# Performance work log

Hardware: AMD Instinct MI355X
Metric: run time of the kernel (lower is better)

Reference implementation:

```python
import jax, jax.numpy as jnp
import numpy as np

N_TOKENS = 16384
D_MODEL = 1024
N_EXPERTS = 4
TOP_K = 2
LN_EPS = 1e-6


def setup_inputs() -> dict:
    key = jax.random.key(0)
    ks = jax.random.split(key, 6)
    d, e = D_MODEL, N_EXPERTS
    return {
        "x": jax.random.normal(ks[0], (N_TOKENS, d), jnp.float32),
        "gate_w": jax.random.normal(ks[1], (e, d), jnp.float32) * (1.0 / np.sqrt(d)),
        "w1": jax.random.normal(ks[2], (e, 2 * d, d), jnp.float32) * (1.0 / np.sqrt(d)),
        "b1": jax.random.normal(ks[3], (e, 2 * d), jnp.float32) * 0.01,
        "w2": jax.random.normal(ks[4], (e, d, 2 * d), jnp.float32) * (1.0 / np.sqrt(2 * d)),
        "b2": jax.random.normal(ks[5], (e, d), jnp.float32) * 0.01,
        "gamma": jnp.ones((e, d), jnp.float32),
        "beta": jnp.zeros((e, d), jnp.float32),
    }


def _expert_ffn(x, w1e, b1e, w2e, b2e, ge, be):
    h = jax.nn.gelu(x @ w1e.T + b1e, approximate=False)   # [N, 2d]
    z = x + (h @ w2e.T + b2e)                              # residual, [N, d]
    mu = jnp.mean(z, axis=-1, keepdims=True)
    var = jnp.var(z, axis=-1, keepdims=True)
    return (z - mu) * jax.lax.rsqrt(var + LN_EPS) * ge + be


def reference(x, gate_w, w1, b1, w2, b2, gamma, beta):
    n = x.shape[0]
    scores = x @ gate_w.T                                  # [N, E]
    ew, ei = jax.lax.top_k(scores, TOP_K)                  # [N, K]
    ew = jax.nn.softmax(ew, axis=-1)
    # combine weights: dense [N, E] routing matrix (each row has K nonzeros)
    comb = jnp.zeros_like(scores).at[jnp.arange(n)[:, None], ei].add(ew)
    y = jnp.zeros_like(x)
    for e in range(N_EXPERTS):  # small fixed expert count
        y = y + comb[:, e:e + 1] * _expert_ffn(x, w1[e], b1[e], w2[e], b2[e], gamma[e], beta[e])
    return y
```

## Files before the change

### kernel.cpp

```cpp
#include <hip/hip_runtime.h>
#include <hip/hip_bf16.h>
#include <math.h>

#define NT 16384
#define DM 1024
#define NE 4

typedef __attribute__((ext_vector_type(8))) short short8;
typedef __attribute__((ext_vector_type(4))) float f32x4;

#define GLDS(g, l)                                                        \
  __builtin_amdgcn_global_load_lds(                                       \
      (const __attribute__((address_space(1))) void*)(g),                 \
      (__attribute__((address_space(3))) void*)(l), 16, 0, 0)

__device__ __forceinline__ float bf2f(short h) {
    union { unsigned u; float f; } v;
    v.u = ((unsigned)(unsigned short)h) << 16;
    return v.f;
}

__global__ __launch_bounds__(256) void detect_kernel(
    const unsigned int* __restrict__ xw, int* __restrict__ flag)
{
    __shared__ int red[4];
    const int t = threadIdx.x;
    int cnt = 0;
    #pragma unroll 4
    for (int i = 0; i < 64; ++i) {
        unsigned w = xw[t * 64 + i];
        unsigned e0 = (w >> 7) & 0xFFu;
        cnt += (e0 >= 100u && e0 <= 150u) ? 1 : 0;
    }
    #pragma unroll
    for (int o = 32; o > 0; o >>= 1) cnt += __shfl_xor(cnt, o);
    if ((t & 63) == 0) red[t >> 6] = cnt;
    __syncthreads();
    if (t == 0) {
        int tot = red[0] + red[1] + red[2] + red[3];
        *flag = (tot > 8192) ? 1 : 0;
    }
}

__global__ __launch_bounds__(256) void init_kernel(
    int* __restrict__ counts, int* __restrict__ idx)
{
    const int t = blockIdx.x * 256 + threadIdx.x;
    idx[t] = 0;
    if (t < NE) counts[t] = 0;
}

__global__ __launch_bounds__(256) void convert_big_kernel(
    const float* __restrict__ src, short* __restrict__ dst, int n,
    const int* __restrict__ flag)
{
    if (*flag) return;
    const int stride = gridDim.x * blockDim.x;
    const int t0 = blockIdx.x * blockDim.x + threadIdx.x;
    const float4* s = (const float4*)src;
    for (int i = t0; i < n / 4; i += stride) {
        float4 v = s[i];
        __hip_bfloat16 b0 = __float2bfloat16(v.x);
        __hip_bfloat16 b1 = __float2bfloat16(v.y);
        __hip_bfloat16 b2 = __float2bfloat16(v.z);
        __hip_bfloat16 b3 = __float2bfloat16(v.w);
        short4 o;
        o.x = *(short*)&b0; o.y = *(short*)&b1;
        o.z = *(short*)&b2; o.w = *(short*)&b3;
        *(short4*)(dst + (size_t)i * 4) = o;
    }
}

__global__ __launch_bounds__(256) void convert_small_kernel(
    const void* __restrict__ b1, const void* __restrict__ b2,
    const void* __restrict__ ga, const void* __restrict__ be,
    short* __restrict__ b1d, short* __restrict__ b2d,
    short* __restrict__ gad, short* __restrict__ bed,
    const int* __restrict__ flag)
{
    const int isbf = *flag;
    const int t = blockIdx.x * 256 + threadIdx.x;
    const void* src; short* dst; int i;
    if (t < 8192)      { src = b1; dst = b1d; i = t; }
    else if (t < 12288){ src = b2; dst = b2d; i = t - 8192; }
    else if (t < 16384){ src = ga; dst = gad; i = t - 12288; }
    else               { src = be; dst = bed; i = t - 16384; }
    short v;
    if (isbf) v = ((const short*)src)[i];
    else {
        __hip_bfloat16 b = __float2bfloat16(((const float*)src)[i]);
        v = *(short*)&b;
    }
    dst[i] = v;
}

__global__ __launch_bounds__(256) void gate_kernel(
    const void* __restrict__ x, const void* __restrict__ gw,
    float* __restrict__ comb, int* __restrict__ choice,
    const int* __restrict__ flag)
{
    const int lane  = threadIdx.x & 63;
    const int token = blockIdx.x * 4 + (threadIdx.x >> 6);
    double s0 = 0., s1 = 0., s2 = 0., s3 = 0.;
    if (*flag) {
        const short8* xr = (const short8*)((const short*)x + (size_t)token * DM);
        const short8* g0 = (const short8*)((const short*)gw + 0 * DM);
        const short8* g1 = (const short8*)((const short*)gw + 1 * DM);
        const short8* g2 = (const short8*)((const short*)gw + 2 * DM);
        const short8* g3 = (const short8*)((const short*)gw + 3 * DM);
        #pragma unroll
        for (int c = 0; c < 2; ++c) {
            short8 xv = xr[c * 64 + lane];
            short8 a0 = g0[c * 64 + lane], a1 = g1[c * 64 + lane];
            short8 a2 = g2[c * 64 + lane], a3 = g3[c * 64 + lane];
            #pragma unroll
            for (int j = 0; j < 8; ++j) {
                double xd = (double)bf2f(xv[j]);
                s0 += xd * (double)bf2f(a0[j]);
                s1 += xd * (double)bf2f(a1[j]);
                s2 += xd * (double)bf2f(a2[j]);
                s3 += xd * (double)bf2f(a3[j]);
            }
        }
    } else {
        const float4* xr = (const float4*)((const float*)x + (size_t)token * DM);
        const float4* g0 = (const float4*)((const float*)gw + 0 * DM);
        const float4* g1 = (const float4*)((const float*)gw + 1 * DM);
        const float4* g2 = (const float4*)((const float*)gw + 2 * DM);
        const float4* g3 = (const float4*)((const float*)gw + 3 * DM);
        #pragma unroll
        for (int c = 0; c < 4; ++c) {
            float4 xv = xr[c * 64 + lane];
            float4 a0 = g0[c * 64 + lane], a1 = g1[c * 64 + lane];
            float4 a2 = g2[c * 64 + lane], a3 = g3[c * 64 + lane];
            s0 += (double)xv.x * a0.x + (double)xv.y * a0.y + (double)xv.z * a0.z + (double)xv.w * a0.w;
            s1 += (double)xv.x * a1.x + (double)xv.y * a1.y + (double)xv.z * a1.z + (double)xv.w * a1.w;
            s2 += (double)xv.x * a2.x + (double)xv.y * a2.y + (double)xv.z * a2.z + (double)xv.w * a2.w;
            s3 += (double)xv.x * a3.x + (double)xv.y * a3.y + (double)xv.z * a3.z + (double)xv.w * a3.w;
        }
    }
    #pragma unroll
    for (int off = 32; off > 0; off >>= 1) {
        s0 += __shfl_xor(s0, off);
        s1 += __shfl_xor(s1, off);
        s2 += __shfl_xor(s2, off);
        s3 += __shfl_xor(s3, off);
    }
    if (lane == 0) {
        double s[4] = {s0, s1, s2, s3};
        int i1 = 0;
        #pragma unroll
        for (int e = 1; e < 4; ++e) if (s[e] > s[i1]) i1 = e;
        int i2 = -1;
        #pragma unroll
        for (int e = 0; e < 4; ++e) {
            if (e == i1) continue;
            if (i2 < 0 || s[e] > s[i2]) i2 = e;
        }
        float e2 = expf((float)(s[i2] - s[i1]));
        float wa = 1.0f / (1.0f + e2);
        float wb = e2 * wa;
        float* cr = comb + (size_t)token * 4;
        #pragma unroll
        for (int e = 0; e < 4; ++e)
            cr[e] = (e == i1) ? wa : ((e == i2) ? wb : 0.0f);
        choice[token] = i1 | (i2 << 8);
    }
}

__global__ __launch_bounds__(256) void route_kernel(
    const int* __restrict__ choice, int* __restrict__ counts,
    int* __restrict__ idx, int* __restrict__ pos)
{
    __shared__ int T[4][8];
    __shared__ int base[4];
    const int tid = threadIdx.x, w = tid >> 6, lane = tid & 63;
    const int t = blockIdx.x * 256 + tid;
    const int c = choice[t];
    const int e0 = c & 0xFF, e1 = (c >> 8) & 0xFF;
    const unsigned long long lt = ((unsigned long long)1 << lane) - 1;
    int rank0 = 0, rank1 = 0;
    #pragma unroll
    for (int e = 0; e < 4; ++e) {
        unsigned long long m0 = __ballot(e0 == e);
        unsigned long long m1 = __ballot(e1 == e);
        if (e0 == e) rank0 = __popcll(m0 & lt);
        if (e1 == e) rank1 = __popcll(m1 & lt);
        if (lane == 0) { T[w][e] = __popcll(m0); T[w][4 + e] = __popcll(m1); }
    }
    __syncthreads();
    if (tid < 4) {
        int tot = 0;
        #pragma unroll
        for (int w2 = 0; w2 < 4; ++w2) tot += T[w2][tid] + T[w2][4 + tid];
        base[tid] = atomicAdd(&counts[tid], tot);
    }
    __syncthreads();
    int off0 = base[e0], off1 = base[e1];
    #pragma unroll
    for (int w2 = 0; w2 < 4; ++w2) {
        if (w2 < w) off0 += T[w2][e0];
        off1 += T[w2][e1];
        if (w2 < w) off1 += T[w2][4 + e1];
    }
    const int p0 = off0 + rank0;
    const int p1 = off1 + rank1;
    idx[e0 * NT + p0] = t;
    idx[e1 * NT + p1] = t;
    pos[t] = p0 | (p1 << 16);
}

template <int EPI, int BM, int BN>
__global__ __launch_bounds__(512, 2) void gemm256(
    const short* __restrict__ Araw, const short* __restrict__ Acvt,
    const short* __restrict__ Braw, const short* __restrict__ Bcvt,
    const short* __restrict__ biasAll,
    void* __restrict__ Cout,
    const int* __restrict__ idxAll,
    const int* __restrict__ counts,
    int c0, int N, int K, const int* __restrict__ flag,
    int eArg, int Rarg)
{
    constexpr int WM = 2, WN = 4;
    constexpr int WTM = BM / WM;
    constexpr int WTN = BN / WN;
    constexpr int MT  = WTM / 16;
    constexpr int NTt = WTN / 16;
    constexpr int ACH = BM / 64;
    constexpr int BCH = BN / 64;
    constexpr int NLD = ACH + BCH;

    const int e    = (Rarg < 0) ? eArg : (int)blockIdx.z;
    const int cnt  = counts[e] - c0;
    const int rowc = (int)blockIdx.y * BM;
    if (rowc >= cnt) return;

    int hRow0 = 0, zRow0 = 0;
    if (Rarg >= 0) {
        hRow0 = e * Rarg;
        int pre = 0;
        #pragma unroll
        for (int i = 0; i < NE; ++i) pre += (i < e) ? counts[i] : 0;
        zRow0 = pre + c0;
    }

    const short* A = (*flag) ? Araw : Acvt;
    const short* B = ((*flag) ? Braw : Bcvt) + (size_t)e * 2 * DM * DM;
    const short* bias = biasAll + (size_t)e * N;

    __shared__ __align__(16) short sA[2][BM * 64];
    __shared__ __align__(16) short sB[2][BN * 64];

    const int tid  = threadIdx.x;
    const int wid  = tid >> 6;
    const int col0 = (int)blockIdx.x * BN;
    const int wm = wid >> 2, wn = wid & 3;
    const int quad = (tid & 63) >> 4;
    const int mrow = tid & 15;

    const int scol = (((tid & 7) ^ ((tid >> 3) & 7)) * 8);
    const short* gA[ACH];
    const short* gB[BCH];
    #pragma unroll
    for (int i = 0; i < ACH; ++i) {
        const int lr = i * 64 + (tid >> 3);
        size_t grow;
        if (EPI == 0) grow = (size_t)idxAll[(size_t)e * NT + c0 + rowc + lr];
        else          grow = (size_t)(hRow0 + rowc + lr);
        gA[i] = A + grow * (size_t)K + scol;
    }
    #pragma unroll
    for (int j = 0; j < BCH; ++j)
        gB[j] = B + (size_t)(col0 + j * 64 + (tid >> 3)) * K + scol;

    f32x4 acc[MT][NTt];
    #pragma unroll
    for (int m = 0; m < MT; ++m)
        #pragma unroll
        for (int n = 0; n < NTt; ++n)
            acc[m][n] = (f32x4){0.f, 0.f, 0.f, 0.f};

    auto stage = [&](int buf, int k0) {
        short* dA = &sA[buf][0] + wid * 512;
        short* dB = &sB[buf][0] + wid * 512;
        #pragma unroll
        for (int i = 0; i < ACH; ++i) GLDS(gA[i] + k0, dA + i * 4096);
        #pragma unroll
        for (int j = 0; j < BCH; ++j) GLDS(gB[j] + k0, dB + j * 4096);
    };

    const int swz  = (mrow & 7) << 4;
    const int boff = (quad * 16) ^ swz;

    const int ntiles = K / 64;
    stage(0, 0);
    int cur = 0;
    for (int t = 0; t < ntiles; ++t) {
        if (t + 1 < ntiles) {
            stage(cur ^ 1, (t + 1) * 64);
            if (NLD == 8)
                asm volatile("s_waitcnt vmcnt(8)" ::: "memory");
            else
                asm volatile("s_waitcnt vmcnt(6)" ::: "memory");
        } else {
            asm volatile("s_waitcnt vmcnt(0)" ::: "memory");
        }
        __builtin_amdgcn_s_barrier();
        __builtin_amdgcn_sched_barrier(0);
        const char* sAc = (const char*)&sA[cur][0];
        const char* sBc = (const char*)&sB[cur][0];
        #pragma unroll
        for (int kk = 0; kk < 64; kk += 32) {
            const int kb = (kk * 2) ^ boff;
            short8 a[MT], b[NTt];
            #pragma unroll
            for (int m = 0; m < MT; ++m) {
                const int R = wm * WTM + m * 16 + mrow;
                a[m] = *(const short8*)(sAc + R * 128 + kb);
            }
            #pragma unroll
            for (int n = 0; n < NTt; ++n) {
                const int R = wn * WTN + n * 16 + mrow;
                b[n] = *(const short8*)(sBc + R * 128 + kb);
            }
            #pragma unroll
            for (int m = 0; m < MT; ++m)
                #pragma unroll
                for (int n = 0; n < NTt; ++n)
                    acc[m][n] = __builtin_amdgcn_mfma_f32_16x16x32_bf16(
                        a[m], b[n], acc[m][n], 0, 0, 0);
        }
        asm volatile("s_waitcnt lgkmcnt(0)" ::: "memory");
        __builtin_amdgcn_sched_barrier(0);
        __builtin_amdgcn_s_barrier();
        cur ^= 1;
    }

    #pragma unroll
    for (int m = 0; m < MT; ++m) {
        #pragma unroll
        for (int n = 0; n < NTt; ++n) {
            const int col = col0 + wn * WTN + n * 16 + mrow;
            const float bval = bf2f(bias[col]);
            #pragma unroll
            for (int i = 0; i < 4; ++i) {
                const int lrow = rowc + wm * WTM + m * 16 + quad * 4 + i;
                if (lrow < cnt) {
                    float v = acc[m][n][i] + bval;
                    if (EPI == 0) {
                        v = 0.5f * v * (1.0f + erff(v * 0.70710678118654752f));
                        ((__hip_bfloat16*)Cout)[(size_t)(hRow0 + lrow) * N + col] =
                            __float2bfloat16(v);
                    } else {
                        ((float*)Cout)[(size_t)(zRow0 + lrow) * N + col] = v;
                    }
                }
            }
        }
    }
}

__global__ __launch_bounds__(256) void ln_fused_kernel(
    const float* __restrict__ z,
    const void* __restrict__ xraw,
    const float* __restrict__ comb,
    const int* __restrict__ choice,
    const int* __restrict__ pos,
    const short* __restrict__ gammaAll,
    const short* __restrict__ betaAll,
    void* __restrict__ y,
    const int* __restrict__ counts, const int* __restrict__ flag)
{
    const int isbf = *flag;
    const int lane = threadIdx.x & 63;
    const int t = blockIdx.x * 4 + (threadIdx.x >> 6);

    const int ca = counts[0], cb = counts[1], cc = counts[2];
    const int ch = choice[t];
    const int e0 = ch & 0xFF, e1 = (ch >> 8) & 0xFF;
    const int pp = pos[t];
    const int p0 = pp & 0xFFFF, p1 = (pp >> 16) & 0xFFFF;
    const int b0r = (e0 > 0 ? ca : 0) + (e0 > 1 ? cb : 0) + (e0 > 2 ? cc : 0);
    const int b1r = (e1 > 0 ? ca : 0) + (e1 > 1 ? cb : 0) + (e1 > 2 ? cc : 0);
    const float w0 = comb[(size_t)t * 4 + e0];
    const float w1 = comb[(size_t)t * 4 + e1];

    const f32x4* z0r = (const f32x4*)(z + (size_t)(b0r + p0) * DM);
    const f32x4* z1r = (const f32x4*)(z + (size_t)(b1r + p1) * DM);

    f32x4 v0[4], v1[4];
    float s0 = 0.f, q0 = 0.f, s1 = 0.f, q1 = 0.f;
    #pragma unroll
    for (int c = 0; c < 4; ++c) {
        f32x4 a = z0r[c * 64 + lane];
        f32x4 b = z1r[c * 64 + lane];
        float xf[4];
        if (isbf) {
            short4 xv = *(const short4*)((const short*)xraw + (size_t)t * DM + c * 256 + lane * 4);
            xf[0] = bf2f(xv.x); xf[1] = bf2f(xv.y); xf[2] = bf2f(xv.z); xf[3] = bf2f(xv.w);
        } else {
            float4 xv = *(const float4*)((const float*)xraw + (size_t)t * DM + c * 256 + lane * 4);
            xf[0] = xv.x; xf[1] = xv.y; xf[2] = xv.z; xf[3] = xv.w;
        }
        #pragma unroll
        for (int j = 0; j < 4; ++j) {
            v0[c][j] = a[j] + xf[j];
            v1[c][j] = b[j] + xf[j];
            s0 += v0[c][j]; q0 += v0[c][j] * v0[c][j];
            s1 += v1[c][j]; q1 += v1[c][j] * v1[c][j];
        }
    }
    #pragma unroll
    for (int o = 32; o > 0; o >>= 1) {
        s0 += __shfl_xor(s0, o); q0 += __shfl_xor(q0, o);
        s1 += __shfl_xor(s1, o); q1 += __shfl_xor(q1, o);
    }
    const float mu0 = s0 * (1.0f / DM);
    const float r0  = rsqrtf(fmaxf(q0 * (1.0f / DM) - mu0 * mu0, 0.0f) + 1e-6f);
    const float mu1 = s1 * (1.0f / DM);
    const float r1  = rsqrtf(fmaxf(q1 * (1.0f / DM) - mu1 * mu1, 0.0f) + 1e-6f);

    #pragma unroll
    for (int c = 0; c < 4; ++c) {
        const int id = c * 256 + lane * 4;
        short4 g0v  = *(const short4*)(gammaAll + (size_t)e0 * DM + id);
        short4 be0v = *(const short4*)(betaAll  + (size_t)e0 * DM + id);
        short4 g1v  = *(const short4*)(gammaAll + (size_t)e1 * DM + id);
        short4 be1v = *(const short4*)(betaAll  + (size_t)e1 * DM + id);
        const float g0f[4]  = {bf2f(g0v.x),  bf2f(g0v.y),  bf2f(g0v.z),  bf2f(g0v.w)};
        const float b0f[4]  = {bf2f(be0v.x), bf2f(be0v.y), bf2f(be0v.z), bf2f(be0v.w)};
        const float g1f[4]  = {bf2f(g1v.x),  bf2f(g1v.y),  bf2f(g1v.z),  bf2f(g1v.w)};
        const float b1f[4]  = {bf2f(be1v.x), bf2f(be1v.y), bf2f(be1v.z), bf2f(be1v.w)};
        float o[4];
        #pragma unroll
        for (int j = 0; j < 4; ++j)
            o[j] = w0 * ((v0[c][j] - mu0) * r0 * g0f[j] + b0f[j])
                 + w1 * ((v1[c][j] - mu1) * r1 * g1f[j] + b1f[j]);
        if (isbf) {
            short4 ov;
            __hip_bfloat16 t0 = __float2bfloat16(o[0]); ov.x = *(short*)&t0;
            __hip_bfloat16 t1 = __float2bfloat16(o[1]); ov.y = *(short*)&t1;
            __hip_bfloat16 t2 = __float2bfloat16(o[2]); ov.z = *(short*)&t2;
            __hip_bfloat16 t3 = __float2bfloat16(o[3]); ov.w = *(short*)&t3;
            *(short4*)((short*)y + (size_t)t * DM + id) = ov;
        } else {
            float4 ov = {o[0], o[1], o[2], o[3]};
            *(float4*)((float*)y + (size_t)t * DM + id) = ov;
        }
    }
}

__global__ __launch_bounds__(256) void ln_kernel(
    const float* __restrict__ z, const void* __restrict__ xraw,
    const float* __restrict__ comb, const int* __restrict__ choice,
    const __hip_bfloat16* __restrict__ gamma,
    const __hip_bfloat16* __restrict__ beta,
    void* __restrict__ y, const int* __restrict__ idxl,
    const int* __restrict__ count, int c0,
    int expert, const int* __restrict__ flag)
{
    const int isbf = *flag;
    const int lane = threadIdx.x & 63;
    const int l    = blockIdx.x * 4 + (threadIdx.x >> 6);
    const int cnt  = *count - c0;
    if (l >= cnt) return;
    const int token = idxl[c0 + l];
    const int ch = choice[token];
    const int e0 = ch & 0xFF, e1 = (ch >> 8) & 0xFF;
    const int firstexp = e0 < e1 ? e0 : e1;
    const int accumulate = (expert != firstexp);

    const f32x4* zr = (const f32x4*)(z + (size_t)l * DM);
    f32x4 v[4];
    float sum = 0.f, ssq = 0.f;
    #pragma unroll
    for (int c = 0; c < 4; ++c) {
        f32x4 zv = zr[c * 64 + lane];
        if (isbf) {
            short4 xv = *(const short4*)((const short*)xraw + (size_t)token * DM + c * 256 + lane * 4);
            v[c][0] = zv[0] + bf2f(xv.x);
            v[c][1] = zv[1] + bf2f(xv.y);
            v[c][2] = zv[2] + bf2f(xv.z);
            v[c][3] = zv[3] + bf2f(xv.w);
        } else {
            float4 xv = *(const float4*)((const float*)xraw + (size_t)token * DM + c * 256 + lane * 4);
            v[c][0] = zv[0] + xv.x;
            v[c][1] = zv[1] + xv.y;
            v[c][2] = zv[2] + xv.z;
            v[c][3] = zv[3] + xv.w;
        }
        #pragma unroll
        for (int j = 0; j < 4; ++j) { sum += v[c][j]; ssq += v[c][j] * v[c][j]; }
    }
    #pragma unroll
    for (int off = 32; off > 0; off >>= 1) {
        sum += __shfl_xor(sum, off);
        ssq += __shfl_xor(ssq, off);
    }
    const float mu   = sum * (1.0f / DM);
    const float var  = fmaxf(ssq * (1.0f / DM) - mu * mu, 0.0f);
    const float rstd = rsqrtf(var + 1e-6f);
    const float w    = comb[(size_t)token * 4 + expert];
    #pragma unroll
    for (int c = 0; c < 4; ++c) {
        #pragma unroll
        for (int j = 0; j < 4; ++j) {
            const int id = c * 256 + lane * 4 + j;
            const float g = __bfloat162float(gamma[id]);
            const float b = __bfloat162float(beta[id]);
            float o = w * ((v[c][j] - mu) * rstd * g + b);
            if (isbf) {
                __hip_bfloat16* yr = (__hip_bfloat16*)y + (size_t)token * DM;
                if (accumulate) o += __bfloat162float(yr[id]);
                yr[id] = __float2bfloat16(o);
            } else {
                float* yr = (float*)y + (size_t)token * DM;
                if (accumulate) o += yr[id];
                yr[id] = o;
            }
        }
    }
}

extern "C" void kernel_launch(void* const* d_in, const int* in_sizes, int n_in,
                              void* d_out, int out_size, void* d_ws, size_t ws_size,
                              hipStream_t stream)
{
    char* ws = (char*)d_ws;
    size_t off = 0;
    auto alloc = [&](size_t bytes) -> char* {
        char* p = ws + off;
        off = (off + bytes + 255) & ~(size_t)255;
        return p;
    };
    int*   flag   = (int*)  alloc(256);
    float* comb   = (float*)alloc((size_t)NT * 4 * sizeof(float));
    int*   choice = (int*)  alloc((size_t)NT * sizeof(int));
    int*   counts = (int*)  alloc(NE * sizeof(int));
    int*   idx    = (int*)  alloc((size_t)NE * NT * sizeof(int));
    int*   pos    = (int*)  alloc((size_t)NT * sizeof(int));
    short* b1b    = (short*)alloc((size_t)NE * 2 * DM * 2);
    short* b2b    = (short*)alloc((size_t)NE * DM * 2);
    short* gb     = (short*)alloc((size_t)NE * DM * 2);
    short* bb     = (short*)alloc((size_t)NE * DM * 2);
    short* w1b    = (short*)alloc((size_t)NE * 2 * DM * DM * 2);
    short* w2b    = (short*)alloc((size_t)NE * 2 * DM * DM * 2);
    short* xb     = (short*)alloc((size_t)NT * DM * 2);
    const size_t fixed = off;

    detect_kernel<<<1, 256, 0, stream>>>((const unsigned int*)d_in[0], flag);
    init_kernel<<<(NE * NT) / 256, 256, 0, stream>>>(counts, idx);

    convert_big_kernel<<<2048, 256, 0, stream>>>((const float*)d_in[0], xb,
                                                 NT * DM, flag);
    convert_big_kernel<<<2048, 256, 0, stream>>>((const float*)d_in[2], w1b,
                                                 NE * 2 * DM * DM, flag);
    convert_big_kernel<<<2048, 256, 0, stream>>>((const float*)d_in[4], w2b,
                                                 NE * 2 * DM * DM, flag);
    convert_small_kernel<<<80, 256, 0, stream>>>(d_in[3], d_in[5], d_in[6], d_in[7],
                                                 b1b, b2b, gb, bb, flag);

    gate_kernel<<<NT / 4, 256, 0, stream>>>(d_in[0], d_in[1], comb, choice, flag);
    route_kernel<<<NT / 256, 256, 0, stream>>>(choice, counts, idx, pos);

    const size_t zBytes = (size_t)2 * NT * DM * sizeof(float);
    int R = 0;
    for (int cand = 2048; cand >= 1024; cand >>= 1) {
        const size_t hBytes = (size_t)NE * cand * 2 * DM * 2;
        if (fixed + hBytes + zBytes + 4096 <= ws_size) { R = cand; break; }
    }

    if (R > 0) {
        short* h = (short*)alloc((size_t)NE * R * 2 * DM * 2);
        float* z = (float*)alloc(zBytes);
        for (int c0 = 0; c0 < NT; c0 += R) {
            dim3 g1(2 * DM / 256, R / 256, NE);
            gemm256<0, 256, 256><<<g1, 512, 0, stream>>>(
                (const short*)d_in[0], xb, (const short*)d_in[2], w1b, b1b,
                (void*)h, idx, counts, c0, 2 * DM, DM, flag, 0, R);
            dim3 g2(DM / 256, R / 128, NE);
            gemm256<1, 128, 256><<<g2, 512, 0, stream>>>(
                h, h, (const short*)d_in[4], w2b, b2b,
                (void*)z, idx, counts, c0, DM, 2 * DM, flag, 0, R);
        }
        ln_fused_kernel<<<NT / 4, 256, 0, stream>>>(z, d_in[0], comb, choice, pos,
                                                    gb, bb, d_out, counts, flag);
    } else {
        int cap = NT;
        while (cap > 512 && fixed + (size_t)cap * 8192 > ws_size) cap >>= 1;
        short* h = (short*)alloc((size_t)cap * 2 * DM * 2);
        float* z = (float*)alloc((size_t)cap * DM * sizeof(float));
        for (int e = 0; e < NE; ++e) {
            for (int c0 = 0; c0 < NT; c0 += cap) {
                dim3 g1(2 * DM / 256, cap / 256, 1);
                gemm256<0, 256, 256><<<g1, 512, 0, stream>>>(
                    (const short*)d_in[0], xb, (const short*)d_in[2], w1b, b1b,
                    (void*)h, idx, counts, c0, 2 * DM, DM, flag, e, -1);
                dim3 g2(DM / 256, cap / 128, 1);
                gemm256<1, 128, 256><<<g2, 512, 0, stream>>>(
                    h, h, (const short*)d_in[4], w2b, b2b,
                    (void*)z, idx, counts, c0, DM, 2 * DM, flag, e, -1);
                ln_kernel<<<cap / 4, 256, 0, stream>>>(z, d_in[0], comb, choice,
                    (const __hip_bfloat16*)(gb + (size_t)e * DM),
                    (const __hip_bfloat16*)(bb + (size_t)e * DM),
                    d_out, idx + (size_t)e * NT, counts + e, c0, e, flag);
            }
        }
    }
}
```

Before: 793.1 us.

## Rework MoE GEMMs with K=32 tiles, XCD remap, single-pass routing and fused converts

The GEMM kernel is rewritten to use a K-step of 32 with a smaller LDS footprint, a fixed 256-row M tile and a new swizzle. Workgroup IDs are remapped across the eight XCDs to improve L2 locality. A new path allocates the full compacted hidden buffer so both expert GEMMs run once over all tokens instead of in chunks, reducing launch count and tail waste. The three fp32-to-bf16 conversion launches are merged into one. The risks are a higher barrier count per K, since each 32-wide tile gets its own sync, and a larger workspace requirement.

Measured after the change: 883.3 us. 11.4% more time.

```diff
diff --git a/kernel.cpp b/kernel.cpp
--- a/kernel.cpp
+++ b/kernel.cpp
@@ -50,16 +50,23 @@
     if (t < NE) counts[t] = 0;
 }
 
-__global__ __launch_bounds__(256) void convert_big_kernel(
-    const float* __restrict__ src, short* __restrict__ dst, int n,
+__global__ __launch_bounds__(256) void convert_all_kernel(
+    const float* __restrict__ x, const float* __restrict__ w1,
+    const float* __restrict__ w2,
+    short* __restrict__ xb, short* __restrict__ w1b, short* __restrict__ w2b,
     const int* __restrict__ flag)
 {
     if (*flag) return;
+    const int n1 = NT * DM / 4;
+    const int n2 = NE * 2 * DM * DM / 4;
+    const int total = n1 + 2 * n2;
     const int stride = gridDim.x * blockDim.x;
-    const int t0 = blockIdx.x * blockDim.x + threadIdx.x;
-    const float4* s = (const float4*)src;
-    for (int i = t0; i < n / 4; i += stride) {
-        float4 v = s[i];
+    for (int i = blockIdx.x * blockDim.x + threadIdx.x; i < total; i += stride) {
+        const float4* s; short* d; int j;
+        if (i < n1)           { s = (const float4*)x;  d = xb;  j = i; }
+        else if (i < n1 + n2) { s = (const float4*)w1; d = w1b; j = i - n1; }
+        else                  { s = (const float4*)w2; d = w2b; j = i - n1 - n2; }
+        float4 v = s[j];
         __hip_bfloat16 b0 = __float2bfloat16(v.x);
         __hip_bfloat16 b1 = __float2bfloat16(v.y);
         __hip_bfloat16 b2 = __float2bfloat16(v.z);
@@ -67,7 +74,7 @@
         short4 o;
         o.x = *(short*)&b0; o.y = *(short*)&b1;
         o.z = *(short*)&b2; o.w = *(short*)&b3;
-        *(short4*)(dst + (size_t)i * 4) = o;
+        *(short4*)(d + (size_t)j * 4) = o;
     }
 }
 
@@ -210,8 +217,8 @@
     pos[t] = p0 | (p1 << 16);
 }
 
-template <int EPI, int BM, int BN>
-__global__ __launch_bounds__(512, 2) void gemm256(
+template <int EPI, int BN>
+__global__ __launch_bounds__(512, 2) void gemm32(
     const short* __restrict__ Araw, const short* __restrict__ Acvt,
     const short* __restrict__ Braw, const short* __restrict__ Bcvt,
     const short* __restrict__ biasAll,
@@ -221,49 +228,61 @@
     int c0, int N, int K, const int* __restrict__ flag,
     int eArg, int Rarg)
 {
-    constexpr int WM = 2, WN = 4;
-    constexpr int WTM = BM / WM;
-    constexpr int WTN = BN / WN;
-    constexpr int MT  = WTM / 16;
+    constexpr int WTM = 128;
+    constexpr int WTN = BN / 4;
+    constexpr int MT  = 8;
     constexpr int NTt = WTN / 16;
-    constexpr int ACH = BM / 64;
-    constexpr int BCH = BN / 64;
-    constexpr int NLD = ACH + BCH;
-
-    const int e    = (Rarg < 0) ? eArg : (int)blockIdx.z;
+    constexpr int BCH = BN / 128;
+
+    int bx, by, bz;
+    {
+        int lid = (int)blockIdx.x +
+                  (int)gridDim.x * ((int)blockIdx.y + (int)gridDim.y * (int)blockIdx.z);
+        const int nwg = (int)(gridDim.x * gridDim.y * gridDim.z);
+        if (Rarg >= 0 && (nwg & 7) == 0) {
+            const int q = nwg >> 3;
+            lid = (lid & 7) * q + (lid >> 3);
+        }
+        bx = lid % (int)gridDim.x;
+        const int rem = lid / (int)gridDim.x;
+        by = rem % (int)gridDim.y;
+        bz = rem / (int)gridDim.y;
+    }
+
+    const int e    = (Rarg < 0) ? eArg : bz;
     const int cnt  = counts[e] - c0;
-    const int rowc = (int)blockIdx.y * BM;
+    const int rowc = by * 256;
     if (rowc >= cnt) return;
 
     int hRow0 = 0, zRow0 = 0;
     if (Rarg >= 0) {
-        hRow0 = e * Rarg;
         int pre = 0;
         #pragma unroll
         for (int i = 0; i < NE; ++i) pre += (i < e) ? counts[i] : 0;
         zRow0 = pre + c0;
+        hRow0 = (Rarg == 0) ? pre : e * Rarg;
     }
 
     const short* A = (*flag) ? Araw : Acvt;
     const short* B = ((*flag) ? Braw : Bcvt) + (size_t)e * 2 * DM * DM;
     const short* bias = biasAll + (size_t)e * N;
 
-    __shared__ __align__(16) short sA[2][BM * 64];
-    __shared__ __align__(16) short sB[2][BN * 64];
+    __shared__ __align__(16) short sA[2][2 * 4096];
+    __shared__ __align__(16) short sB[2][BCH * 4096];
 
     const int tid  = threadIdx.x;
     const int wid  = tid >> 6;
-    const int col0 = (int)blockIdx.x * BN;
+    const int col0 = bx * BN;
     const int wm = wid >> 2, wn = wid & 3;
     const int quad = (tid & 63) >> 4;
     const int mrow = tid & 15;
 
-    const int scol = (((tid & 7) ^ ((tid >> 3) & 7)) * 8);
-    const short* gA[ACH];
+    const int scol = (((tid & 3) ^ ((tid >> 3) & 3)) * 8);
+    const short* gA[2];
     const short* gB[BCH];
     #pragma unroll
-    for (int i = 0; i < ACH; ++i) {
-        const int lr = i * 64 + (tid >> 3);
+    for (int i = 0; i < 2; ++i) {
+        const int lr = i * 128 + (tid >> 2);
         size_t grow;
         if (EPI == 0) grow = (size_t)idxAll[(size_t)e * NT + c0 + rowc + lr];
         else          grow = (size_t)(hRow0 + rowc + lr);
@@ -271,7 +290,7 @@
     }
     #pragma unroll
     for (int j = 0; j < BCH; ++j)
-        gB[j] = B + (size_t)(col0 + j * 64 + (tid >> 3)) * K + scol;
+        gB[j] = B + (size_t)(col0 + j * 128 + (tid >> 2)) * K + scol;
 
     f32x4 acc[MT][NTt];
     #pragma unroll
@@ -281,55 +300,44 @@
             acc[m][n] = (f32x4){0.f, 0.f, 0.f, 0.f};
 
     auto stage = [&](int buf, int k0) {
-        short* dA = &sA[buf][0] + wid * 512;
-        short* dB = &sB[buf][0] + wid * 512;
-        #pragma unroll
-        for (int i = 0; i < ACH; ++i) GLDS(gA[i] + k0, dA + i * 4096);
-        #pragma unroll
-        for (int j = 0; j < BCH; ++j) GLDS(gB[j] + k0, dB + j * 4096);
+        #pragma unroll
+        for (int i = 0; i < 2; ++i)   GLDS(gA[i] + k0, &sA[buf][i * 4096] + wid * 512);
+        #pragma unroll
+        for (int j = 0; j < BCH; ++j) GLDS(gB[j] + k0, &sB[buf][j * 4096] + wid * 512);
     };
 
-    const int swz  = (mrow & 7) << 4;
-    const int boff = (quad * 16) ^ swz;
-
-    const int ntiles = K / 64;
+    const int boff = ((quad ^ ((mrow >> 1) & 3)) << 4);
+
+    const int ntiles = K / 32;
     stage(0, 0);
     int cur = 0;
     for (int t = 0; t < ntiles; ++t) {
         if (t + 1 < ntiles) {
-            stage(cur ^ 1, (t + 1) * 64);
-            if (NLD == 8)
-                asm volatile("s_waitcnt vmcnt(8)" ::: "memory");
+            stage(cur ^ 1, (t + 1) * 32);
+            if (BCH == 2)
+                asm volatile("s_waitcnt vmcnt(4)" ::: "memory");
             else
-                asm volatile("s_waitcnt vmcnt(6)" ::: "memory");
+                asm volatile("s_waitcnt vmcnt(3)" ::: "memory");
         } else {
             asm volatile("s_waitcnt vmcnt(0)" ::: "memory");
         }
+        __builtin_amdgcn_sched_barrier(0);
         __builtin_amdgcn_s_barrier();
-        __builtin_amdgcn_sched_barrier(0);
         const char* sAc = (const char*)&sA[cur][0];
         const char* sBc = (const char*)&sB[cur][0];
-        #pragma unroll
-        for (int kk = 0; kk < 64; kk += 32) {
-            const int kb = (kk * 2) ^ boff;
-            short8 a[MT], b[NTt];
+        short8 a[MT], b[NTt];
+        #pragma unroll
+        for (int m = 0; m < MT; ++m)
+            a[m] = *(const short8*)(sAc + (wm * WTM + m * 16 + mrow) * 64 + boff);
+        #pragma unroll
+        for (int n = 0; n < NTt; ++n)
+            b[n] = *(const short8*)(sBc + (wn * WTN + n * 16 + mrow) * 64 + boff);
+        #pragma unroll
+        for (int m = 0; m < MT; ++m)
             #pragma unroll
-            for (int m = 0; m < MT; ++m) {
-                const int R = wm * WTM + m * 16 + mrow;
-                a[m] = *(const short8*)(sAc + R * 128 + kb);
-            }
-            #pragma unroll
-            for (int n = 0; n < NTt; ++n) {
-                const int R = wn * WTN + n * 16 + mrow;
-                b[n] = *(const short8*)(sBc + R * 128 + kb);
-            }
-            #pragma unroll
-            for (int m = 0; m < MT; ++m)
-                #pragma unroll
-                for (int n = 0; n < NTt; ++n)
-                    acc[m][n] = __builtin_amdgcn_mfma_f32_16x16x32_bf16(
-                        a[m], b[n], acc[m][n], 0, 0, 0);
-        }
+            for (int n = 0; n < NTt; ++n)
+                acc[m][n] = __builtin_amdgcn_mfma_f32_16x16x32_bf16(
+                    a[m], b[n], acc[m][n], 0, 0, 0);
         asm volatile("s_waitcnt lgkmcnt(0)" ::: "memory");
         __builtin_amdgcn_sched_barrier(0);
         __builtin_amdgcn_s_barrier();
@@ -551,12 +559,9 @@
     detect_kernel<<<1, 256, 0, stream>>>((const unsigned int*)d_in[0], flag);
     init_kernel<<<(NE * NT) / 256, 256, 0, stream>>>(counts, idx);
 
-    convert_big_kernel<<<2048, 256, 0, stream>>>((const float*)d_in[0], xb,
-                                                 NT * DM, flag);
-    convert_big_kernel<<<2048, 256, 0, stream>>>((const float*)d_in[2], w1b,
-                                                 NE * 2 * DM * DM, flag);
-    convert_big_kernel<<<2048, 256, 0, stream>>>((const float*)d_in[4], w2b,
-                                                 NE * 2 * DM * DM, flag);
+    convert_all_kernel<<<2048, 256, 0, stream>>>(
+        (const float*)d_in[0], (const float*)d_in[2], (const float*)d_in[4],
+        xb, w1b, w2b, flag);
     convert_small_kernel<<<80, 256, 0, stream>>>(d_in[3], d_in[5], d_in[6], d_in[7],
                                                  b1b, b2b, gb, bb, flag);
 
@@ -564,8 +569,26 @@
     route_kernel<<<NT / 256, 256, 0, stream>>>(choice, counts, idx, pos);
 
     const size_t zBytes = (size_t)2 * NT * DM * sizeof(float);
+    const size_t hFull  = (size_t)(2 * NT + 256) * (2 * DM) * 2;
+
+    if (fixed + hFull + zBytes + 4096 <= ws_size) {
+        short* h = (short*)alloc(hFull);
+        float* z = (float*)alloc(zBytes);
+        dim3 g1(2 * DM / 256, NT / 256, NE);
+        gemm32<0, 256><<<g1, 512, 0, stream>>>(
+            (const short*)d_in[0], xb, (const short*)d_in[2], w1b, b1b,
+            (void*)h, idx, counts, 0, 2 * DM, DM, flag, 0, 0);
+        dim3 g2(DM / 128, NT / 256, NE);
+        gemm32<1, 128><<<g2, 512, 0, stream>>>(
+            h, h, (const short*)d_in[4], w2b, b2b,
+            (void*)z, idx, counts, 0, DM, 2 * DM, flag, 0, 0);
+        ln_fused_kernel<<<NT / 4, 256, 0, stream>>>(z, d_in[0], comb, choice, pos,
+                                                    gb, bb, d_out, counts, flag);
+        return;
+    }
+
     int R = 0;
-    for (int cand = 2048; cand >= 1024; cand >>= 1) {
+    for (int cand = 4096; cand >= 1024; cand >>= 1) {
         const size_t hBytes = (size_t)NE * cand * 2 * DM * 2;
         if (fixed + hBytes + zBytes + 4096 <= ws_size) { R = cand; break; }
     }
@@ -575,11 +598,11 @@
         float* z = (float*)alloc(zBytes);
         for (int c0 = 0; c0 < NT; c0 += R) {
             dim3 g1(2 * DM / 256, R / 256, NE);
-            gemm256<0, 256, 256><<<g1, 512, 0, stream>>>(
+            gemm32<0, 256><<<g1, 512, 0, stream>>>(
                 (const short*)d_in[0], xb, (const short*)d_in[2], w1b, b1b,
                 (void*)h, idx, counts, c0, 2 * DM, DM, flag, 0, R);
-            dim3 g2(DM / 256, R / 128, NE);
-            gemm256<1, 128, 256><<<g2, 512, 0, stream>>>(
+            dim3 g2(DM / 128, R / 256, NE);
+            gemm32<1, 128><<<g2, 512, 0, stream>>>(
                 h, h, (const short*)d_in[4], w2b, b2b,
                 (void*)z, idx, counts, c0, DM, 2 * DM, flag, 0, R);
         }
@@ -593,11 +616,11 @@
         for (int e = 0; e < NE; ++e) {
             for (int c0 = 0; c0 < NT; c0 += cap) {
                 dim3 g1(2 * DM / 256, cap / 256, 1);
-                gemm256<0, 256, 256><<<g1, 512, 0, stream>>>(
+                gemm32<0, 256><<<g1, 512, 0, stream>>>(
                     (const short*)d_in[0], xb, (const short*)d_in[2], w1b, b1b,
                     (void*)h, idx, counts, c0, 2 * DM, DM, flag, e, -1);
-                dim3 g2(DM / 256, cap / 128, 1);
-                gemm256<1, 128, 256><<<g2, 512, 0, stream>>>(
+                dim3 g2(DM / 128, cap / 256, 1);
+                gemm32<1, 128><<<g2, 512, 0, stream>>>(
                     h, h, (const short*)d_in[4], w2b, b2b,
                     (void*)z, idx, counts, c0, DM, 2 * DM, flag, e, -1);
                 ln_kernel<<<cap / 4, 256, 0, stream>>>(z, d_in[0], comb, choice,
```
